# Performance work log

Measured on AMD Instinct MI355X. Metric: run time of the kernel, lower is better.

Reference implementation:

```python
import jax, jax.numpy as jnp
import numpy as np

NUM_PITCHES = 88
H_FEAT = 188
LSTM_UNITS = 48
N_STATES = 5
CTX_HID = 16
CTX_OUT = 4


def _glorot(key, shape):
    fan_in, fan_out = shape[1], shape[0]
    lim = (6.0 / (fan_in + fan_out)) ** 0.5
    return jax.random.uniform(key, shape, jnp.float32, -lim, lim)


def setup_inputs() -> dict:
    key = jax.random.key(0)
    ks = jax.random.split(key, 16)
    B, T = 16, 256
    pitch_features = jax.random.normal(ks[0], (B, NUM_PITCHES, H_FEAT, T), jnp.float32)
    prev_context = jax.random.uniform(ks[1], (B, NUM_PITCHES, 3), jnp.float32)
    # context net params
    fc1_w = _glorot(ks[2], (CTX_HID, 3)); fc1_b = jnp.zeros((CTX_HID,), jnp.float32)
    fc2_w = _glorot(ks[3], (CTX_HID, CTX_HID)); fc2_b = jnp.zeros((CTX_HID,), jnp.float32)
    fc3_w = _glorot(ks[4], (CTX_OUT, CTX_HID)); fc3_b = jnp.zeros((CTX_OUT,), jnp.float32)
    # lstm1: input H_FEAT+4 -> 48; gates order i,f,g,o (torch convention)
    in1 = H_FEAT + CTX_OUT
    lstm1_wih = _glorot(ks[5], (4 * LSTM_UNITS, in1))
    lstm1_whh = _glorot(ks[6], (4 * LSTM_UNITS, LSTM_UNITS))
    lstm1_bih = jnp.zeros((4 * LSTM_UNITS,), jnp.float32)
    lstm1_bhh = jnp.zeros((4 * LSTM_UNITS,), jnp.float32)
    lstm2_wih = _glorot(ks[7], (4 * LSTM_UNITS, LSTM_UNITS))
    lstm2_whh = _glorot(ks[8], (4 * LSTM_UNITS, LSTM_UNITS))
    lstm2_bih = jnp.zeros((4 * LSTM_UNITS,), jnp.float32)
    lstm2_bhh = jnp.zeros((4 * LSTM_UNITS,), jnp.float32)
    fc_states_w = _glorot(ks[9], (N_STATES, LSTM_UNITS))
    fc_states_b = jnp.zeros((N_STATES,), jnp.float32)
    return dict(pitch_features=pitch_features, prev_context=prev_context,
                fc1_w=fc1_w, fc1_b=fc1_b, fc2_w=fc2_w, fc2_b=fc2_b,
                fc3_w=fc3_w, fc3_b=fc3_b,
                lstm1_wih=lstm1_wih, lstm1_whh=lstm1_whh, lstm1_bih=lstm1_bih, lstm1_bhh=lstm1_bhh,
                lstm2_wih=lstm2_wih, lstm2_whh=lstm2_whh, lstm2_bih=lstm2_bih, lstm2_bhh=lstm2_bhh,
                fc_states_w=fc_states_w, fc_states_b=fc_states_b)


def _lstm_scan(x, wih, whh, bih, bhh):
    # x: (S, N, In); zero init state; returns (S, N, U)
    S, N, _ = x.shape
    U = whh.shape[1]
    xg = jnp.einsum('sni,gi->sng', x, wih) + bih + bhh  # precompute input gates

    def step(carry, xg_t):
        h, c = carry
        g = xg_t + h @ whh.T  # (N, 4U)
        i, f, gg, o = jnp.split(g, 4, axis=-1)
        c = jax.nn.sigmoid(f) * c + jax.nn.sigmoid(i) * jnp.tanh(gg)
        h = jax.nn.sigmoid(o) * jnp.tanh(c)
        return (h, c), h

    init = (jnp.zeros((N, U), x.dtype), jnp.zeros((N, U), x.dtype))
    _, hs = jax.lax.scan(step, init, xg)
    return hs


def reference(pitch_features, prev_context,
              fc1_w, fc1_b, fc2_w, fc2_b, fc3_w, fc3_b,
              lstm1_wih, lstm1_whh, lstm1_bih, lstm1_bhh,
              lstm2_wih, lstm2_whh, lstm2_bih, lstm2_bhh,
              fc_states_w, fc_states_b):
    B, P, H, T = pitch_features.shape
    # Context net (context never updates across t in the original loop)
    x = jax.nn.relu(prev_context @ fc1_w.T + fc1_b)
    x = jax.nn.relu(x @ fc2_w.T + fc2_b)
    ctx_emb = x @ fc3_w.T + fc3_b  # (B, P, 4)
    # Each timestep t is independent: LSTM runs over the pitch axis (len 88)
    # with zero initial state every step. Fold (B, T) into batch N.
    pf = jnp.transpose(pitch_features, (1, 0, 3, 2)).reshape(P, B * T, H)  # (P, BT, H)
    ce = jnp.broadcast_to(ctx_emb[:, None, :, :], (B, T, P, CTX_OUT))
    ce = jnp.transpose(ce, (2, 0, 1, 3)).reshape(P, B * T, CTX_OUT)
    seq = jnp.concatenate([pf, ce], axis=-1)  # (P, BT, H+4)
    h = _lstm_scan(seq, lstm1_wih, lstm1_whh, lstm1_bih, lstm1_bhh)
    h = _lstm_scan(h, lstm2_wih, lstm2_whh, lstm2_bih, lstm2_bhh)
    logits = h @ fc_states_w.T + fc_states_b  # (P, BT, 5)
    logits = logits.reshape(P, B, T, N_STATES)
    logits = jnp.transpose(logits, (1, 0, 3, 2))  # (B, P, 5, T)
    return jax.nn.softmax(logits, axis=2)
```

## Files before the change

### kernel.cpp

```cpp
#include <hip/hip_runtime.h>
#include <hip/hip_bf16.h>
#include <cstdint>

#define P_ 88
#define B_ 16
#define T_ 256
#define H_ 188
#define G_ 192
#define U_ 48
#define N_ 4096

typedef __attribute__((ext_vector_type(8))) short bf16x8;
typedef __attribute__((ext_vector_type(8))) _Float16 f16x8;
typedef __attribute__((ext_vector_type(4))) float f32x4;

__device__ __forceinline__ float sigf(float x) {
  return __builtin_amdgcn_rcpf(1.0f + __expf(-x));
}
__device__ __forceinline__ float tanh_f(float x) {
  return 1.0f - 2.0f * __builtin_amdgcn_rcpf(1.0f + __expf(2.0f * x));
}
__device__ __forceinline__ unsigned short f2bs(float v) {
  union { __hip_bfloat16 h; unsigned short s; } u;
  u.h = __float2bfloat16(v);
  return u.s;
}
__device__ __forceinline__ float bs2f(unsigned short s) {
  union { unsigned int u; float f; } x;
  x.u = ((unsigned int)s) << 16;
  return x.f;
}
__device__ __forceinline__ float hs2f(unsigned short s) {
  union { unsigned short u; _Float16 h; } x;
  x.u = s;
  return (float)x.h;
}
__device__ __forceinline__ unsigned short f2hs(float v) {
  union { _Float16 h; unsigned short s; } x;
  x.h = (_Float16)v;
  return x.s;
}

__device__ __forceinline__ void lds_barrier() {
  asm volatile("s_waitcnt lgkmcnt(0)\n\ts_barrier" ::: "memory");
}

__global__ void ctx_kernel(const float* __restrict__ pc,
                           const float* __restrict__ fc1w, const float* __restrict__ fc1b,
                           const float* __restrict__ fc2w, const float* __restrict__ fc2b,
                           const float* __restrict__ fc3w, const float* __restrict__ fc3b,
                           const float* __restrict__ wih1,
                           const float* __restrict__ bih1, const float* __restrict__ bhh1,
                           float* __restrict__ ctxg) {
  int bp = blockIdx.x * 64 + threadIdx.x;
  if (bp >= B_ * P_) return;
  float p0 = pc[bp * 3 + 0], p1 = pc[bp * 3 + 1], p2 = pc[bp * 3 + 2];
  float x1[16], x2[16];
#pragma unroll
  for (int jj = 0; jj < 16; ++jj)
    x1[jj] = fmaxf(0.f, fc1w[jj * 3 + 0] * p0 + fc1w[jj * 3 + 1] * p1 + fc1w[jj * 3 + 2] * p2 + fc1b[jj]);
#pragma unroll
  for (int jj = 0; jj < 16; ++jj) {
    float s = fc2b[jj];
#pragma unroll
    for (int i = 0; i < 16; ++i) s += fc2w[jj * 16 + i] * x1[i];
    x2[jj] = fmaxf(0.f, s);
  }
  float ce[4];
#pragma unroll
  for (int jj = 0; jj < 4; ++jj) {
    float s = fc3b[jj];
#pragma unroll
    for (int i = 0; i < 16; ++i) s += fc3w[jj * 16 + i] * x2[i];
    ce[jj] = s;
  }
  float* op = ctxg + (size_t)bp * G_;
  for (int g = 0; g < G_; ++g) {
    const float* wr = wih1 + (size_t)g * G_ + H_;
    op[g] = bih1[g] + bhh1[g] + ce[0] * wr[0] + ce[1] * wr[1] + ce[2] * wr[2] + ce[3] * wr[3];
  }
}

__global__ __launch_bounds__(256) void wfrag_kernel(const float* __restrict__ wih1,
                                                    f16x8* __restrict__ wfrag) {
  const int idx = blockIdx.x * 256 + threadIdx.x;
  if (idx >= 12 * 6 * 64) return;
  const int l = idx & 63;
  const int kc = (idx >> 6) % 6;
  const int j = idx / 384;
  const int g = j * 16 + (l & 15);
  const int k0 = kc * 32 + (l >> 4) * 8;
  f16x8 v;
#pragma unroll
  for (int e = 0; e < 8; ++e) {
    const int k = k0 + e;
    const float wv = (k < H_) ? wih1[(size_t)g * G_ + k] : 0.f;
    v[e] = (_Float16)wv;
  }
  wfrag[idx] = v;
}

__global__ __launch_bounds__(256, 3) void gemm_mfma(const float* __restrict__ pf,
                                                    const f16x8* __restrict__ wfrag,
                                                    const float* __restrict__ ctxg,
                                                    unsigned short* __restrict__ xg2) {
  const int bp = blockIdx.x >> 1, tb = blockIdx.x & 1;
  const int p = bp % P_, b = bp / P_;
  const int tid = threadIdx.x;
  const int w = tid >> 6, l = tid & 63;
  const int lj = l & 15, lq = l >> 4;

  __shared__ __align__(16) char ldsraw[49152];
  _Float16(*Ahi)[34] = (_Float16(*)[34])ldsraw;
  _Float16(*Alo)[34] = (_Float16(*)[34])(ldsraw + 8704);

  float cg[12];
#pragma unroll
  for (int jn = 0; jn < 12; ++jn)
    cg[jn] = ctxg[(size_t)bp * G_ + jn * 16 + lj];

  f32x4 acc[2][12];
#pragma unroll
  for (int mt = 0; mt < 2; ++mt)
#pragma unroll
    for (int jn = 0; jn < 12; ++jn)
#pragma unroll
      for (int r = 0; r < 4; ++r) acc[mt][jn][r] = 0.f;

  const float* Ab = pf + (size_t)bp * H_ * T_ + tb * 128;
  const int kl = tid >> 5;
  const int t4 = (tid & 31) * 4;

  for (int kc = 0; kc < 6; ++kc) {
    __syncthreads();
#pragma unroll
    for (int rr = 0; rr < 4; ++rr) {
      const int kk = rr * 8 + kl;
      const int kg = kc * 32 + kk;
      float a0 = 0.f, a1 = 0.f, a2 = 0.f, a3 = 0.f;
      if (kg < H_) {
        const float4 v = *(const float4*)(Ab + (size_t)kg * T_ + t4);
        a0 = v.x; a1 = v.y; a2 = v.z; a3 = v.w;
      }
      const _Float16 h0 = (_Float16)a0, h1 = (_Float16)a1;
      const _Float16 h2 = (_Float16)a2, h3 = (_Float16)a3;
      Ahi[t4 + 0][kk] = h0; Alo[t4 + 0][kk] = (_Float16)(a0 - (float)h0);
      Ahi[t4 + 1][kk] = h1; Alo[t4 + 1][kk] = (_Float16)(a1 - (float)h1);
      Ahi[t4 + 2][kk] = h2; Alo[t4 + 2][kk] = (_Float16)(a2 - (float)h2);
      Ahi[t4 + 3][kk] = h3; Alo[t4 + 3][kk] = (_Float16)(a3 - (float)h3);
    }
    __syncthreads();
    const int trow = w * 32;
    const f16x8 ahi0 = *(const f16x8*)&Ahi[trow + lj][lq * 8];
    const f16x8 ahi1 = *(const f16x8*)&Ahi[trow + 16 + lj][lq * 8];
    const f16x8 alo0 = *(const f16x8*)&Alo[trow + lj][lq * 8];
    const f16x8 alo1 = *(const f16x8*)&Alo[trow + 16 + lj][lq * 8];
#pragma unroll
    for (int jn = 0; jn < 12; ++jn) {
      const f16x8 wf = wfrag[(jn * 6 + kc) * 64 + l];
      acc[0][jn] = __builtin_amdgcn_mfma_f32_16x16x32_f16(ahi0, wf, acc[0][jn], 0, 0, 0);
      acc[1][jn] = __builtin_amdgcn_mfma_f32_16x16x32_f16(ahi1, wf, acc[1][jn], 0, 0, 0);
      acc[0][jn] = __builtin_amdgcn_mfma_f32_16x16x32_f16(alo0, wf, acc[0][jn], 0, 0, 0);
      acc[1][jn] = __builtin_amdgcn_mfma_f32_16x16x32_f16(alo1, wf, acc[1][jn], 0, 0, 0);
    }
  }
  __syncthreads();

  unsigned short* Cst = (unsigned short*)ldsraw + w * 6144;
#pragma unroll
  for (int mt = 0; mt < 2; ++mt)
#pragma unroll
    for (int jn = 0; jn < 12; ++jn)
#pragma unroll
      for (int r = 0; r < 4; ++r)
        Cst[mt * 3072 + jn * 256 + r * 64 + l] = f2hs(acc[mt][jn][r] + cg[jn]);
  const int nb0 = b * 16 + tb * 8 + w * 2;
  unsigned short* gb = xg2 + ((size_t)p * 256 + nb0) * 3072;
#pragma unroll
  for (int rr = 0; rr < 12; ++rr) {
    const uint4 v = *(const uint4*)(Cst + rr * 512 + l * 8);
    *(uint4*)(gb + rr * 512 + l * 8) = v;
  }
}

__global__ __launch_bounds__(256, 2) void scan_mfma(
    const unsigned short* __restrict__ xg2,
    const float* __restrict__ whh1, const float* __restrict__ wih2,
    const float* __restrict__ whh2, const float* __restrict__ bih2,
    const float* __restrict__ bhh2, const float* __restrict__ fcw,
    const float* __restrict__ fcb, float* __restrict__ out) {
  __shared__ __align__(16) short hh[16][104];
  __shared__ __align__(16) short hl[16][104];
  __shared__ __align__(16) float gs[8][196];
  __shared__ __align__(16) float h2f[8][52];
  __shared__ __align__(16) float fcws[5 * 48];
  __shared__ float logit_s[5][8];
  __shared__ float prob_s[5][8];

  const int tid = threadIdx.x;
  const int w = tid >> 6;
  const int l = tid & 63;
  const int lj = l & 15;
  const int lq = l >> 4;
  const int grp = blockIdx.x >> 1;
  const int half = blockIdx.x & 1;
  const int n0 = blockIdx.x * 8;
  const int b = n0 >> 8, t0 = n0 & 255;

  bf16x8 b1[3][2];
  bf16x8 b2f[3][3];
  float bias2r[3];
#pragma unroll
  for (int i = 0; i < 3; ++i) {
    const int j = w * 48 + i * 16 + lj;
    bias2r[i] = bih2[j] + bhh2[j];
#pragma unroll
    for (int kc = 0; kc < 2; ++kc)
#pragma unroll
      for (int e = 0; e < 8; ++e) {
        const int u = kc * 32 + lq * 8 + e;
        b1[i][kc][e] = (u < U_) ? (short)f2bs(whh1[j * U_ + u]) : (short)0;
      }
#pragma unroll
    for (int kc = 0; kc < 3; ++kc)
#pragma unroll
      for (int e = 0; e < 8; ++e) {
        const int u = kc * 32 + lq * 8 + e;
        b2f[i][kc][e] = (u < U_) ? (short)f2bs(wih2[j * U_ + u])
                                 : (short)f2bs(whh2[j * U_ + (u - U_)]);
      }
  }

  for (int e = tid; e < 16 * 104 / 2; e += 256) {
    ((unsigned int*)hh)[e] = 0u;
    ((unsigned int*)hl)[e] = 0u;
  }
  for (int e = tid; e < 5 * U_; e += 256) fcws[e] = fcw[e];

  const int tn0 = tid / U_, tu0 = tid % U_;
  const int tn1 = (256 + tid) / U_, tu1 = (256 + tid) % U_;
  float c1r[2] = {0.f, 0.f}, c2r[2] = {0.f, 0.f};
  const bool fcth = tid < 40;
  const int fk = tid >> 3, fn = tid & 7;
  const float fcbr = fcth ? fcb[fk] : 0.f;
  const int sk = (tid - 96) >> 3, sn = (tid - 96) & 7;

  unsigned short xp[12];
  {
    const size_t pb = (size_t)grp * 3072;
#pragma unroll
    for (int i = 0; i < 3; ++i)
#pragma unroll
      for (int r = 0; r < 4; ++r)
        xp[i * 4 + r] = (lq < 2)
            ? xg2[pb + (size_t)((w * 3 + i) * 256 + r * 64 + (half * 2 + lq) * 16 + lj)]
            : (unsigned short)0;
  }
  const short* hhrow = &hh[lj][0];
  const short* hlrow = &hl[lj][0];
  lds_barrier();

  for (int p = 0; p < P_; ++p) {
    f32x4 cH[3], cL[3];
#pragma unroll
    for (int i = 0; i < 3; ++i)
#pragma unroll
      for (int r = 0; r < 4; ++r) { cH[i][r] = hs2f(xp[i * 4 + r]); cL[i][r] = 0.f; }
    if (p < P_ - 1) {
      const size_t pb = (size_t)((p + 1) * 256 + grp) * 3072;
#pragma unroll
      for (int i = 0; i < 3; ++i)
#pragma unroll
        for (int r = 0; r < 4; ++r)
          xp[i * 4 + r] = (lq < 2)
              ? xg2[pb + (size_t)((w * 3 + i) * 256 + r * 64 + (half * 2 + lq) * 16 + lj)]
              : (unsigned short)0;
    }
    {
      bf16x8 ah0 = *(const bf16x8*)(hhrow + lq * 8);
      bf16x8 ah1 = *(const bf16x8*)(hhrow + 32 + lq * 8);
      bf16x8 al0 = *(const bf16x8*)(hlrow + lq * 8);
      bf16x8 al1 = *(const bf16x8*)(hlrow + 32 + lq * 8);
#pragma unroll
      for (int i = 0; i < 3; ++i)
        cH[i] = __builtin_amdgcn_mfma_f32_16x16x32_bf16(ah0, b1[i][0], cH[i], 0, 0, 0);
#pragma unroll
      for (int i = 0; i < 3; ++i)
        cL[i] = __builtin_amdgcn_mfma_f32_16x16x32_bf16(al0, b1[i][0], cL[i], 0, 0, 0);
#pragma unroll
      for (int i = 0; i < 3; ++i)
        cH[i] = __builtin_amdgcn_mfma_f32_16x16x32_bf16(ah1, b1[i][1], cH[i], 0, 0, 0);
#pragma unroll
      for (int i = 0; i < 3; ++i)
        cL[i] = __builtin_amdgcn_mfma_f32_16x16x32_bf16(al1, b1[i][1], cL[i], 0, 0, 0);
    }
    if (lq < 2) {
#pragma unroll
      for (int i = 0; i < 3; ++i)
#pragma unroll
        for (int r = 0; r < 4; ++r)
          gs[lq * 4 + r][w * 48 + i * 16 + lj] = cH[i][r] + cL[i][r];
    }
    if (p > 0 && fcth) {
      float a = fcbr;
#pragma unroll
      for (int uq = 0; uq < 12; ++uq) {
        f32x4 hv = *(const f32x4*)&h2f[fn][uq * 4];
        f32x4 wv = *(const f32x4*)&fcws[fk * 48 + uq * 4];
        a += hv[0] * wv[0] + hv[1] * wv[1] + hv[2] * wv[2] + hv[3] * wv[3];
      }
      logit_s[fk][fn] = a;
    }
    lds_barrier();
    {
      const int n = tn0, u = tu0;
      const float ig = gs[n][u], fg = gs[n][48 + u];
      const float gg = gs[n][96 + u], og = gs[n][144 + u];
      const float cc = sigf(fg) * c1r[0] + sigf(ig) * tanh_f(gg);
      c1r[0] = cc;
      const float h = sigf(og) * tanh_f(cc);
      const unsigned short hb = f2bs(h);
      hh[n][u] = (short)hb;
      hl[n][u] = (short)f2bs(h - bs2f(hb));
    }
    if (tid < 128) {
      const int n = tn1, u = tu1;
      const float ig = gs[n][u], fg = gs[n][48 + u];
      const float gg = gs[n][96 + u], og = gs[n][144 + u];
      const float cc = sigf(fg) * c1r[1] + sigf(ig) * tanh_f(gg);
      c1r[1] = cc;
      const float h = sigf(og) * tanh_f(cc);
      const unsigned short hb = f2bs(h);
      hh[n][u] = (short)hb;
      hl[n][u] = (short)f2bs(h - bs2f(hb));
    }
    if (p > 0 && tid >= 192 && tid < 200) {
      const int n = tid - 192;
      const float l0 = logit_s[0][n], l1 = logit_s[1][n], l2 = logit_s[2][n],
                  l3 = logit_s[3][n], l4 = logit_s[4][n];
      const float m = fmaxf(fmaxf(fmaxf(l0, l1), fmaxf(l2, l3)), l4);
      const float e0 = __expf(l0 - m), e1 = __expf(l1 - m), e2 = __expf(l2 - m),
                  e3 = __expf(l3 - m), e4 = __expf(l4 - m);
      const float rs = __builtin_amdgcn_rcpf(e0 + e1 + e2 + e3 + e4);
      prob_s[0][n] = e0 * rs; prob_s[1][n] = e1 * rs; prob_s[2][n] = e2 * rs;
      prob_s[3][n] = e3 * rs; prob_s[4][n] = e4 * rs;
    }
    lds_barrier();
    f32x4 c2H[3], c2L[3];
#pragma unroll
    for (int i = 0; i < 3; ++i) {
      c2H[i][0] = bias2r[i]; c2H[i][1] = bias2r[i];
      c2H[i][2] = bias2r[i]; c2H[i][3] = bias2r[i];
      c2L[i][0] = 0.f; c2L[i][1] = 0.f; c2L[i][2] = 0.f; c2L[i][3] = 0.f;
    }
    {
      bf16x8 a0 = *(const bf16x8*)(hhrow + lq * 8);
      bf16x8 a1 = *(const bf16x8*)(hhrow + 32 + lq * 8);
      bf16x8 a2 = *(const bf16x8*)(hhrow + 64 + lq * 8);
      bf16x8 q0 = *(const bf16x8*)(hlrow + lq * 8);
      bf16x8 q1 = *(const bf16x8*)(hlrow + 32 + lq * 8);
      bf16x8 q2 = *(const bf16x8*)(hlrow + 64 + lq * 8);
#pragma unroll
      for (int i = 0; i < 3; ++i)
        c2H[i] = __builtin_amdgcn_mfma_f32_16x16x32_bf16(a0, b2f[i][0], c2H[i], 0, 0, 0);
#pragma unroll
      for (int i = 0; i < 3; ++i)
        c2L[i] = __builtin_amdgcn_mfma_f32_16x16x32_bf16(q0, b2f[i][0], c2L[i], 0, 0, 0);
#pragma unroll
      for (int i = 0; i < 3; ++i)
        c2H[i] = __builtin_amdgcn_mfma_f32_16x16x32_bf16(a1, b2f[i][1], c2H[i], 0, 0, 0);
#pragma unroll
      for (int i = 0; i < 3; ++i)
        c2L[i] = __builtin_amdgcn_mfma_f32_16x16x32_bf16(q1, b2f[i][1], c2L[i], 0, 0, 0);
#pragma unroll
      for (int i = 0; i < 3; ++i)
        c2H[i] = __builtin_amdgcn_mfma_f32_16x16x32_bf16(a2, b2f[i][2], c2H[i], 0, 0, 0);
#pragma unroll
      for (int i = 0; i < 3; ++i)
        c2L[i] = __builtin_amdgcn_mfma_f32_16x16x32_bf16(q2, b2f[i][2], c2L[i], 0, 0, 0);
    }
    if (lq < 2) {
#pragma unroll
      for (int i = 0; i < 3; ++i)
#pragma unroll
        for (int r = 0; r < 4; ++r)
          gs[lq * 4 + r][w * 48 + i * 16 + lj] = c2H[i][r] + c2L[i][r];
    }
    if (p > 0 && tid >= 96 && tid < 136) {
      out[(((size_t)b * P_ + (p - 1)) * 5 + sk) * T_ + t0 + sn] = prob_s[sk][sn];
    }
    lds_barrier();
    {
      const int n = tn0, u = tu0;
      const float ig = gs[n][u], fg = gs[n][48 + u];
      const float gg = gs[n][96 + u], og = gs[n][144 + u];
      const float cc = sigf(fg) * c2r[0] + sigf(ig) * tanh_f(gg);
      c2r[0] = cc;
      const float h = sigf(og) * tanh_f(cc);
      const unsigned short hb = f2bs(h);
      hh[n][48 + u] = (short)hb;
      hl[n][48 + u] = (short)f2bs(h - bs2f(hb));
      h2f[n][u] = h;
    }
    if (tid < 128) {
      const int n = tn1, u = tu1;
      const float ig = gs[n][u], fg = gs[n][48 + u];
      const float gg = gs[n][96 + u], og = gs[n][144 + u];
      const float cc = sigf(fg) * c2r[1] + sigf(ig) * tanh_f(gg);
      c2r[1] = cc;
      const float h = sigf(og) * tanh_f(cc);
      const unsigned short hb = f2bs(h);
      hh[n][48 + u] = (short)hb;
      hl[n][48 + u] = (short)f2bs(h - bs2f(hb));
      h2f[n][u] = h;
    }
    lds_barrier();
  }
  if (fcth) {
    float a = fcbr;
#pragma unroll
    for (int uq = 0; uq < 12; ++uq) {
      f32x4 hv = *(const f32x4*)&h2f[fn][uq * 4];
      f32x4 wv = *(const f32x4*)&fcws[fk * 48 + uq * 4];
      a += hv[0] * wv[0] + hv[1] * wv[1] + hv[2] * wv[2] + hv[3] * wv[3];
    }
    logit_s[fk][fn] = a;
  }
  lds_barrier();
  if (tid >= 192 && tid < 200) {
    const int n = tid - 192;
    const float l0 = logit_s[0][n], l1 = logit_s[1][n], l2 = logit_s[2][n],
                l3 = logit_s[3][n], l4 = logit_s[4][n];
    const float m = fmaxf(fmaxf(fmaxf(l0, l1), fmaxf(l2, l3)), l4);
    const float e0 = __expf(l0 - m), e1 = __expf(l1 - m), e2 = __expf(l2 - m),
                e3 = __expf(l3 - m), e4 = __expf(l4 - m);
    const float rs = __builtin_amdgcn_rcpf(e0 + e1 + e2 + e3 + e4);
    prob_s[0][n] = e0 * rs; prob_s[1][n] = e1 * rs; prob_s[2][n] = e2 * rs;
    prob_s[3][n] = e3 * rs; prob_s[4][n] = e4 * rs;
  }
  lds_barrier();
  if (tid >= 96 && tid < 136) {
    out[(((size_t)b * P_ + (P_ - 1)) * 5 + sk) * T_ + t0 + sn] = prob_s[sk][sn];
  }
}

extern "C" void kernel_launch(void* const* d_in, const int* in_sizes, int n_in,
                              void* d_out, int out_size, void* d_ws, size_t ws_size,
                              hipStream_t stream) {
  const float* pf   = (const float*)d_in[0];
  const float* pc   = (const float*)d_in[1];
  const float* fc1w = (const float*)d_in[2];
  const float* fc1b = (const float*)d_in[3];
  const float* fc2w = (const float*)d_in[4];
  const float* fc2b = (const float*)d_in[5];
  const float* fc3w = (const float*)d_in[6];
  const float* fc3b = (const float*)d_in[7];
  const float* wih1 = (const float*)d_in[8];
  const float* whh1 = (const float*)d_in[9];
  const float* bih1 = (const float*)d_in[10];
  const float* bhh1 = (const float*)d_in[11];
  const float* wih2 = (const float*)d_in[12];
  const float* whh2 = (const float*)d_in[13];
  const float* bih2 = (const float*)d_in[14];
  const float* bhh2 = (const float*)d_in[15];
  const float* fcw  = (const float*)d_in[16];
  const float* fcb  = (const float*)d_in[17];
  float* out = (float*)d_out;

  char* wsp = (char*)d_ws;
  float* ctxg = (float*)wsp;
  const size_t CTXG_BYTES = (size_t)B_ * P_ * G_ * sizeof(float);
  f16x8* wfrag = (f16x8*)(wsp + CTXG_BYTES);
  const size_t WFRAG_BYTES = (size_t)12 * 6 * 64 * 16;
  unsigned short* xg2 = (unsigned short*)(wsp + CTXG_BYTES + WFRAG_BYTES);

  ctx_kernel<<<22, 64, 0, stream>>>(pc, fc1w, fc1b, fc2w, fc2b, fc3w, fc3b,
                                    wih1, bih1, bhh1, ctxg);
  wfrag_kernel<<<18, 256, 0, stream>>>(wih1, wfrag);
  gemm_mfma<<<B_ * P_ * 2, 256, 0, stream>>>(pf, wfrag, ctxg, xg2);
  scan_mfma<<<N_ / 8, 256, 0, stream>>>(xg2, whh1, wih2, whh2,
                                        bih2, bhh2, fcw, fcb, out);
}
```

Measured before the change: 413.2 us.

## Process two 8-sequence groups per scan block to interleave independent recurrences

```diff
diff --git a/kernel.cpp b/kernel.cpp
--- a/kernel.cpp
+++ b/kernel.cpp
@@ -39,6 +39,14 @@
   union { _Float16 h; unsigned short s; } x;
   x.h = (_Float16)v;
   return x.s;
+}
+__device__ __forceinline__ void hsplit(float h, unsigned short& hi, unsigned short& lo) {
+  union { float f; unsigned int u; } x;
+  x.f = h;
+  hi = (unsigned short)(x.u >> 16);
+  union { float f; unsigned int u; } y;
+  y.f = h - bs2f(hi);
+  lo = (unsigned short)(y.u >> 16);
 }
 
 __device__ __forceinline__ void lds_barrier() {
@@ -183,28 +191,27 @@
   }
 }
 
-__global__ __launch_bounds__(256, 2) void scan_mfma(
+__global__ __launch_bounds__(256, 1) void scan_mfma(
     const unsigned short* __restrict__ xg2,
     const float* __restrict__ whh1, const float* __restrict__ wih2,
     const float* __restrict__ whh2, const float* __restrict__ bih2,
     const float* __restrict__ bhh2, const float* __restrict__ fcw,
     const float* __restrict__ fcb, float* __restrict__ out) {
-  __shared__ __align__(16) short hh[16][104];
-  __shared__ __align__(16) short hl[16][104];
-  __shared__ __align__(16) float gs[8][196];
-  __shared__ __align__(16) float h2f[8][52];
+  __shared__ __align__(16) short hhX[16][104], hlX[16][104];
+  __shared__ __align__(16) short hhY[16][104], hlY[16][104];
+  __shared__ __align__(16) float gsX[8][196], gsY[8][196];
+  __shared__ __align__(16) float h2fX[8][52], h2fY[8][52];
   __shared__ __align__(16) float fcws[5 * 48];
-  __shared__ float logit_s[5][8];
-  __shared__ float prob_s[5][8];
+  __shared__ float logitX[5][8], probX[5][8];
+  __shared__ float logitY[5][8], probY[5][8];
 
   const int tid = threadIdx.x;
   const int w = tid >> 6;
   const int l = tid & 63;
   const int lj = l & 15;
   const int lq = l >> 4;
-  const int grp = blockIdx.x >> 1;
-  const int half = blockIdx.x & 1;
-  const int n0 = blockIdx.x * 8;
+  const int grp = blockIdx.x;
+  const int n0 = grp * 16;
   const int b = n0 >> 8, t0 = n0 & 255;
 
   bf16x8 b1[3][2];
@@ -232,215 +239,360 @@
   }
 
   for (int e = tid; e < 16 * 104 / 2; e += 256) {
-    ((unsigned int*)hh)[e] = 0u;
-    ((unsigned int*)hl)[e] = 0u;
+    ((unsigned int*)hhX)[e] = 0u; ((unsigned int*)hlX)[e] = 0u;
+    ((unsigned int*)hhY)[e] = 0u; ((unsigned int*)hlY)[e] = 0u;
   }
   for (int e = tid; e < 5 * U_; e += 256) fcws[e] = fcw[e];
 
   const int tn0 = tid / U_, tu0 = tid % U_;
   const int tn1 = (256 + tid) / U_, tu1 = (256 + tid) % U_;
-  float c1r[2] = {0.f, 0.f}, c2r[2] = {0.f, 0.f};
-  const bool fcth = tid < 40;
-  const int fk = tid >> 3, fn = tid & 7;
-  const float fcbr = fcth ? fcb[fk] : 0.f;
-  const int sk = (tid - 96) >> 3, sn = (tid - 96) & 7;
-
-  unsigned short xp[12];
+  float c1X[2] = {0.f, 0.f}, c1Y[2] = {0.f, 0.f};
+  float c2X[2] = {0.f, 0.f}, c2Y[2] = {0.f, 0.f};
+
+  const bool fcXth = tid < 40, fcYth = tid >= 40 && tid < 80;
+  const int fi = fcXth ? tid : (tid - 40);
+  const int fk = fi >> 3, fn = fi & 7;
+  const float fcbr = (fcXth || fcYth) ? fcb[fk] : 0.f;
+  const bool stXth = tid >= 96 && tid < 136, stYth = tid >= 136 && tid < 176;
+  const int si = stXth ? (tid - 96) : (tid - 136);
+  const int sk = si >> 3, sn = si & 7;
+  const bool smXth = tid >= 192 && tid < 200, smYth = tid >= 200 && tid < 208;
+  const int smn = smXth ? (tid - 192) : (tid - 200);
+
+  unsigned short xpX[12], xpY[12];
   {
     const size_t pb = (size_t)grp * 3072;
 #pragma unroll
     for (int i = 0; i < 3; ++i)
 #pragma unroll
-      for (int r = 0; r < 4; ++r)
-        xp[i * 4 + r] = (lq < 2)
-            ? xg2[pb + (size_t)((w * 3 + i) * 256 + r * 64 + (half * 2 + lq) * 16 + lj)]
-            : (unsigned short)0;
-  }
-  const short* hhrow = &hh[lj][0];
-  const short* hlrow = &hl[lj][0];
+      for (int r = 0; r < 4; ++r) {
+        const size_t base = pb + (size_t)((w * 3 + i) * 256 + r * 64);
+        xpX[i * 4 + r] = (lq < 2) ? xg2[base + lq * 16 + lj] : (unsigned short)0;
+        xpY[i * 4 + r] = (lq < 2) ? xg2[base + (2 + lq) * 16 + lj] : (unsigned short)0;
+      }
+  }
   lds_barrier();
 
   for (int p = 0; p < P_; ++p) {
-    f32x4 cH[3], cL[3];
+    f32x4 cHX[3], cLX[3], cHY[3], cLY[3];
 #pragma unroll
     for (int i = 0; i < 3; ++i)
 #pragma unroll
-      for (int r = 0; r < 4; ++r) { cH[i][r] = hs2f(xp[i * 4 + r]); cL[i][r] = 0.f; }
+      for (int r = 0; r < 4; ++r) {
+        cHX[i][r] = hs2f(xpX[i * 4 + r]); cLX[i][r] = 0.f;
+        cHY[i][r] = hs2f(xpY[i * 4 + r]); cLY[i][r] = 0.f;
+      }
     if (p < P_ - 1) {
       const size_t pb = (size_t)((p + 1) * 256 + grp) * 3072;
 #pragma unroll
       for (int i = 0; i < 3; ++i)
 #pragma unroll
-        for (int r = 0; r < 4; ++r)
-          xp[i * 4 + r] = (lq < 2)
-              ? xg2[pb + (size_t)((w * 3 + i) * 256 + r * 64 + (half * 2 + lq) * 16 + lj)]
-              : (unsigned short)0;
+        for (int r = 0; r < 4; ++r) {
+          const size_t base = pb + (size_t)((w * 3 + i) * 256 + r * 64);
+          xpX[i * 4 + r] = (lq < 2) ? xg2[base + lq * 16 + lj] : (unsigned short)0;
+          xpY[i * 4 + r] = (lq < 2) ? xg2[base + (2 + lq) * 16 + lj] : (unsigned short)0;
+        }
     }
     {
-      bf16x8 ah0 = *(const bf16x8*)(hhrow + lq * 8);
-      bf16x8 ah1 = *(const bf16x8*)(hhrow + 32 + lq * 8);
-      bf16x8 al0 = *(const bf16x8*)(hlrow + lq * 8);
-      bf16x8 al1 = *(const bf16x8*)(hlrow + 32 + lq * 8);
+      const short* hrX = &hhX[lj][0];
+      const short* lrX = &hlX[lj][0];
+      const short* hrY = &hhY[lj][0];
+      const short* lrY = &hlY[lj][0];
+      bf16x8 xa0 = *(const bf16x8*)(hrX + lq * 8);
+      bf16x8 xa1 = *(const bf16x8*)(hrX + 32 + lq * 8);
+      bf16x8 xl0 = *(const bf16x8*)(lrX + lq * 8);
+      bf16x8 xl1 = *(const bf16x8*)(lrX + 32 + lq * 8);
+      bf16x8 ya0 = *(const bf16x8*)(hrY + lq * 8);
+      bf16x8 ya1 = *(const bf16x8*)(hrY + 32 + lq * 8);
+      bf16x8 yl0 = *(const bf16x8*)(lrY + lq * 8);
+      bf16x8 yl1 = *(const bf16x8*)(lrY + 32 + lq * 8);
+#pragma unroll
+      for (int i = 0; i < 3; ++i) {
+        cHX[i] = __builtin_amdgcn_mfma_f32_16x16x32_bf16(xa0, b1[i][0], cHX[i], 0, 0, 0);
+        cHY[i] = __builtin_amdgcn_mfma_f32_16x16x32_bf16(ya0, b1[i][0], cHY[i], 0, 0, 0);
+      }
+#pragma unroll
+      for (int i = 0; i < 3; ++i) {
+        cLX[i] = __builtin_amdgcn_mfma_f32_16x16x32_bf16(xl0, b1[i][0], cLX[i], 0, 0, 0);
+        cLY[i] = __builtin_amdgcn_mfma_f32_16x16x32_bf16(yl0, b1[i][0], cLY[i], 0, 0, 0);
+      }
+#pragma unroll
+      for (int i = 0; i < 3; ++i) {
+        cHX[i] = __builtin_amdgcn_mfma_f32_16x16x32_bf16(xa1, b1[i][1], cHX[i], 0, 0, 0);
+        cHY[i] = __builtin_amdgcn_mfma_f32_16x16x32_bf16(ya1, b1[i][1], cHY[i], 0, 0, 0);
+      }
+#pragma unroll
+      for (int i = 0; i < 3; ++i) {
+        cLX[i] = __builtin_amdgcn_mfma_f32_16x16x32_bf16(xl1, b1[i][1], cLX[i], 0, 0, 0);
+        cLY[i] = __builtin_amdgcn_mfma_f32_16x16x32_bf16(yl1, b1[i][1], cLY[i], 0, 0, 0);
+      }
+    }
+    if (lq < 2) {
 #pragma unroll
       for (int i = 0; i < 3; ++i)
-        cH[i] = __builtin_amdgcn_mfma_f32_16x16x32_bf16(ah0, b1[i][0], cH[i], 0, 0, 0);
-#pragma unroll
-      for (int i = 0; i < 3; ++i)
-        cL[i] = __builtin_amdgcn_mfma_f32_16x16x32_bf16(al0, b1[i][0], cL[i], 0, 0, 0);
-#pragma unroll
-      for (int i = 0; i < 3; ++i)
-        cH[i] = __builtin_amdgcn_mfma_f32_16x16x32_bf16(ah1, b1[i][1], cH[i], 0, 0, 0);
-#pragma unroll
-      for (int i = 0; i < 3; ++i)
-        cL[i] = __builtin_amdgcn_mfma_f32_16x16x32_bf16(al1, b1[i][1], cL[i], 0, 0, 0);
-    }
-    if (lq < 2) {
-#pragma unroll
-      for (int i = 0; i < 3; ++i)
-#pragma unroll
-        for (int r = 0; r < 4; ++r)
-          gs[lq * 4 + r][w * 48 + i * 16 + lj] = cH[i][r] + cL[i][r];
-    }
-    if (p > 0 && fcth) {
+#pragma unroll
+        for (int r = 0; r < 4; ++r) {
+          gsX[lq * 4 + r][w * 48 + i * 16 + lj] = cHX[i][r] + cLX[i][r];
+          gsY[lq * 4 + r][w * 48 + i * 16 + lj] = cHY[i][r] + cLY[i][r];
+        }
+    }
+    if (p > 0 && fcXth) {
       float a = fcbr;
 #pragma unroll
       for (int uq = 0; uq < 12; ++uq) {
-        f32x4 hv = *(const f32x4*)&h2f[fn][uq * 4];
+        f32x4 hv = *(const f32x4*)&h2fX[fn][uq * 4];
         f32x4 wv = *(const f32x4*)&fcws[fk * 48 + uq * 4];
         a += hv[0] * wv[0] + hv[1] * wv[1] + hv[2] * wv[2] + hv[3] * wv[3];
       }
-      logit_s[fk][fn] = a;
+      logitX[fk][fn] = a;
+    }
+    if (p > 0 && fcYth) {
+      float a = fcbr;
+#pragma unroll
+      for (int uq = 0; uq < 12; ++uq) {
+        f32x4 hv = *(const f32x4*)&h2fY[fn][uq * 4];
+        f32x4 wv = *(const f32x4*)&fcws[fk * 48 + uq * 4];
+        a += hv[0] * wv[0] + hv[1] * wv[1] + hv[2] * wv[2] + hv[3] * wv[3];
+      }
+      logitY[fk][fn] = a;
     }
     lds_barrier();
     {
       const int n = tn0, u = tu0;
-      const float ig = gs[n][u], fg = gs[n][48 + u];
-      const float gg = gs[n][96 + u], og = gs[n][144 + u];
-      const float cc = sigf(fg) * c1r[0] + sigf(ig) * tanh_f(gg);
-      c1r[0] = cc;
-      const float h = sigf(og) * tanh_f(cc);
-      const unsigned short hb = f2bs(h);
-      hh[n][u] = (short)hb;
-      hl[n][u] = (short)f2bs(h - bs2f(hb));
+      {
+        const float ig = gsX[n][u], fg = gsX[n][48 + u];
+        const float gg = gsX[n][96 + u], og = gsX[n][144 + u];
+        const float cc = sigf(fg) * c1X[0] + sigf(ig) * tanh_f(gg);
+        c1X[0] = cc;
+        const float h = sigf(og) * tanh_f(cc);
+        unsigned short hb, lb; hsplit(h, hb, lb);
+        hhX[n][u] = (short)hb; hlX[n][u] = (short)lb;
+      }
+      {
+        const float ig = gsY[n][u], fg = gsY[n][48 + u];
+        const float gg = gsY[n][96 + u], og = gsY[n][144 + u];
+        const float cc = sigf(fg) * c1Y[0] + sigf(ig) * tanh_f(gg);
+        c1Y[0] = cc;
+        const float h = sigf(og) * tanh_f(cc);
+        unsigned short hb, lb; hsplit(h, hb, lb);
+        hhY[n][u] = (short)hb; hlY[n][u] = (short)lb;
+      }
     }
     if (tid < 128) {
       const int n = tn1, u = tu1;
-      const float ig = gs[n][u], fg = gs[n][48 + u];
-      const float gg = gs[n][96 + u], og = gs[n][144 + u];
-      const float cc = sigf(fg) * c1r[1] + sigf(ig) * tanh_f(gg);
-      c1r[1] = cc;
-      const float h = sigf(og) * tanh_f(cc);
-      const unsigned short hb = f2bs(h);
-      hh[n][u] = (short)hb;
-      hl[n][u] = (short)f2bs(h - bs2f(hb));
-    }
-    if (p > 0 && tid >= 192 && tid < 200) {
-      const int n = tid - 192;
-      const float l0 = logit_s[0][n], l1 = logit_s[1][n], l2 = logit_s[2][n],
-                  l3 = logit_s[3][n], l4 = logit_s[4][n];
+      {
+        const float ig = gsX[n][u], fg = gsX[n][48 + u];
+        const float gg = gsX[n][96 + u], og = gsX[n][144 + u];
+        const float cc = sigf(fg) * c1X[1] + sigf(ig) * tanh_f(gg);
+        c1X[1] = cc;
+        const float h = sigf(og) * tanh_f(cc);
+        unsigned short hb, lb; hsplit(h, hb, lb);
+        hhX[n][u] = (short)hb; hlX[n][u] = (short)lb;
+      }
+      {
+        const float ig = gsY[n][u], fg = gsY[n][48 + u];
+        const float gg = gsY[n][96 + u], og = gsY[n][144 + u];
+        const float cc = sigf(fg) * c1Y[1] + sigf(ig) * tanh_f(gg);
+        c1Y[1] = cc;
+        const float h = sigf(og) * tanh_f(cc);
+        unsigned short hb, lb; hsplit(h, hb, lb);
+        hhY[n][u] = (short)hb; hlY[n][u] = (short)lb;
+      }
+    }
+    if (p > 0 && smXth) {
+      const int n = smn;
+      const float l0 = logitX[0][n], l1 = logitX[1][n], l2 = logitX[2][n],
+                  l3 = logitX[3][n], l4 = logitX[4][n];
       const float m = fmaxf(fmaxf(fmaxf(l0, l1), fmaxf(l2, l3)), l4);
       const float e0 = __expf(l0 - m), e1 = __expf(l1 - m), e2 = __expf(l2 - m),
                   e3 = __expf(l3 - m), e4 = __expf(l4 - m);
       const float rs = __builtin_amdgcn_rcpf(e0 + e1 + e2 + e3 + e4);
-      prob_s[0][n] = e0 * rs; prob_s[1][n] = e1 * rs; prob_s[2][n] = e2 * rs;
-      prob_s[3][n] = e3 * rs; prob_s[4][n] = e4 * rs;
+      probX[0][n] = e0 * rs; probX[1][n] = e1 * rs; probX[2][n] = e2 * rs;
+      probX[3][n] = e3 * rs; probX[4][n] = e4 * rs;
+    }
+    if (p > 0 && smYth) {
+      const int n = smn;
+      const float l0 = logitY[0][n], l1 = logitY[1][n], l2 = logitY[2][n],
+                  l3 = logitY[3][n], l4 = logitY[4][n];
+      const float m = fmaxf(fmaxf(fmaxf(l0, l1), fmaxf(l2, l3)), l4);
+      const float e0 = __expf(l0 - m), e1 = __expf(l1 - m), e2 = __expf(l2 - m),
+                  e3 = __expf(l3 - m), e4 = __expf(l4 - m);
+      const float rs = __builtin_amdgcn_rcpf(e0 + e1 + e2 + e3 + e4);
+      probY[0][n] = e0 * rs; probY[1][n] = e1 * rs; probY[2][n] = e2 * rs;
+      probY[3][n] = e3 * rs; probY[4][n] = e4 * rs;
     }
     lds_barrier();
-    f32x4 c2H[3], c2L[3];
+    f32x4 dHX[3], dLX[3], dHY[3], dLY[3];
 #pragma unroll
     for (int i = 0; i < 3; ++i) {
-      c2H[i][0] = bias2r[i]; c2H[i][1] = bias2r[i];
-      c2H[i][2] = bias2r[i]; c2H[i][3] = bias2r[i];
-      c2L[i][0] = 0.f; c2L[i][1] = 0.f; c2L[i][2] = 0.f; c2L[i][3] = 0.f;
+      dHX[i][0] = bias2r[i]; dHX[i][1] = bias2r[i];
+      dHX[i][2] = bias2r[i]; dHX[i][3] = bias2r[i];
+      dHY[i][0] = bias2r[i]; dHY[i][1] = bias2r[i];
+      dHY[i][2] = bias2r[i]; dHY[i][3] = bias2r[i];
+      dLX[i][0] = 0.f; dLX[i][1] = 0.f; dLX[i][2] = 0.f; dLX[i][3] = 0.f;
+      dLY[i][0] = 0.f; dLY[i][1] = 0.f; dLY[i][2] = 0.f; dLY[i][3] = 0.f;
     }
     {
-      bf16x8 a0 = *(const bf16x8*)(hhrow + lq * 8);
-      bf16x8 a1 = *(const bf16x8*)(hhrow + 32 + lq * 8);
-      bf16x8 a2 = *(const bf16x8*)(hhrow + 64 + lq * 8);
-      bf16x8 q0 = *(const bf16x8*)(hlrow + lq * 8);
-      bf16x8 q1 = *(const bf16x8*)(hlrow + 32 + lq * 8);
-      bf16x8 q2 = *(const bf16x8*)(hlrow + 64 + lq * 8);
+      const short* hrX = &hhX[lj][0];
+      const short* lrX = &hlX[lj][0];
+      const short* hrY = &hhY[lj][0];
+      const short* lrY = &hlY[lj][0];
+      bf16x8 xa0 = *(const bf16x8*)(hrX + lq * 8);
+      bf16x8 xa1 = *(const bf16x8*)(hrX + 32 + lq * 8);
+      bf16x8 xa2 = *(const bf16x8*)(hrX + 64 + lq * 8);
+      bf16x8 xq0 = *(const bf16x8*)(lrX + lq * 8);
+      bf16x8 xq1 = *(const bf16x8*)(lrX + 32 + lq * 8);
+      bf16x8 xq2 = *(const bf16x8*)(lrX + 64 + lq * 8);
+      bf16x8 ya0 = *(const bf16x8*)(hrY + lq * 8);
+      bf16x8 ya1 = *(const bf16x8*)(hrY + 32 + lq * 8);
+      bf16x8 ya2 = *(const bf16x8*)(hrY + 64 + lq * 8);
+      bf16x8 yq0 = *(const bf16x8*)(lrY + lq * 8);
+      bf16x8 yq1 = *(const bf16x8*)(lrY + 32 + lq * 8);
+      bf16x8 yq2 = *(const bf16x8*)(lrY + 64 + lq * 8);
+#pragma unroll
+      for (int i = 0; i < 3; ++i) {
+        dHX[i] = __builtin_amdgcn_mfma_f32_16x16x32_bf16(xa0, b2f[i][0], dHX[i], 0, 0, 0);
+        dHY[i] = __builtin_amdgcn_mfma_f32_16x16x32_bf16(ya0, b2f[i][0], dHY[i], 0, 0, 0);
+      }
+#pragma unroll
+      for (int i = 0; i < 3; ++i) {
+        dLX[i] = __builtin_amdgcn_mfma_f32_16x16x32_bf16(xq0, b2f[i][0], dLX[i], 0, 0, 0);
+        dLY[i] = __builtin_amdgcn_mfma_f32_16x16x32_bf16(yq0, b2f[i][0], dLY[i], 0, 0, 0);
+      }
+#pragma unroll
+      for (int i = 0; i < 3; ++i) {
+        dHX[i] = __builtin_amdgcn_mfma_f32_16x16x32_bf16(xa1, b2f[i][1], dHX[i], 0, 0, 0);
+        dHY[i] = __builtin_amdgcn_mfma_f32_16x16x32_bf16(ya1, b2f[i][1], dHY[i], 0, 0, 0);
+      }
+#pragma unroll
+      for (int i = 0; i < 3; ++i) {
+        dLX[i] = __builtin_amdgcn_mfma_f32_16x16x32_bf16(xq1, b2f[i][1], dLX[i], 0, 0, 0);
+        dLY[i] = __builtin_amdgcn_mfma_f32_16x16x32_bf16(yq1, b2f[i][1], dLY[i], 0, 0, 0);
+      }
+#pragma unroll
+      for (int i = 0; i < 3; ++i) {
+        dHX[i] = __builtin_amdgcn_mfma_f32_16x16x32_bf16(xa2, b2f[i][2], dHX[i], 0, 0, 0);
+        dHY[i] = __builtin_amdgcn_mfma_f32_16x16x32_bf16(ya2, b2f[i][2], dHY[i], 0, 0, 0);
+      }
+#pragma unroll
+      for (int i = 0; i < 3; ++i) {
+        dLX[i] = __builtin_amdgcn_mfma_f32_16x16x32_bf16(xq2, b2f[i][2], dLX[i], 0, 0, 0);
+        dLY[i] = __builtin_amdgcn_mfma_f32_16x16x32_bf16(yq2, b2f[i][2], dLY[i], 0, 0, 0);
+      }
+    }
+    if (lq < 2) {
 #pragma unroll
       for (int i = 0; i < 3; ++i)
-        c2H[i] = __builtin_amdgcn_mfma_f32_16x16x32_bf16(a0, b2f[i][0], c2H[i], 0, 0, 0);
-#pragma unroll
-      for (int i = 0; i < 3; ++i)
-        c2L[i] = __builtin_amdgcn_mfma_f32_16x16x32_bf16(q0, b2f[i][0], c2L[i], 0, 0, 0);
-#pragma unroll
-      for (int i = 0; i < 3; ++i)
-        c2H[i] = __builtin_amdgcn_mfma_f32_16x16x32_bf16(a1, b2f[i][1], c2H[i], 0, 0, 0);
-#pragma unroll
-      for (int i = 0; i < 3; ++i)
-        c2L[i] = __builtin_amdgcn_mfma_f32_16x16x32_bf16(q1, b2f[i][1], c2L[i], 0, 0, 0);
-#pragma unroll
-      for (int i = 0; i < 3; ++i)
-        c2H[i] = __builtin_amdgcn_mfma_f32_16x16x32_bf16(a2, b2f[i][2], c2H[i], 0, 0, 0);
-#pragma unroll
-      for (int i = 0; i < 3; ++i)
-        c2L[i] = __builtin_amdgcn_mfma_f32_16x16x32_bf16(q2, b2f[i][2], c2L[i], 0, 0, 0);
-    }
-    if (lq < 2) {
-#pragma unroll
-      for (int i = 0; i < 3; ++i)
-#pragma unroll
-        for (int r = 0; r < 4; ++r)
-          gs[lq * 4 + r][w * 48 + i * 16 + lj] = c2H[i][r] + c2L[i][r];
-    }
-    if (p > 0 && tid >= 96 && tid < 136) {
-      out[(((size_t)b * P_ + (p - 1)) * 5 + sk) * T_ + t0 + sn] = prob_s[sk][sn];
+#pragma unroll
+        for (int r = 0; r < 4; ++r) {
+          gsX[lq * 4 + r][w * 48 + i * 16 + lj] = dHX[i][r] + dLX[i][r];
+          gsY[lq * 4 + r][w * 48 + i * 16 + lj] = dHY[i][r] + dLY[i][r];
+        }
+    }
+    if (p > 0 && stXth) {
+      out[(((size_t)b * P_ + (p - 1)) * 5 + sk) * T_ + t0 + sn] = probX[sk][sn];
+    }
+    if (p > 0 && stYth) {
+      out[(((size_t)b * P_ + (p - 1)) * 5 + sk) * T_ + t0 + 8 + sn] = probY[sk][sn];
     }
     lds_barrier();
     {
       const int n = tn0, u = tu0;
-      const float ig = gs[n][u], fg = gs[n][48 + u];
-      const float gg = gs[n][96 + u], og = gs[n][144 + u];
-      const float cc = sigf(fg) * c2r[0] + sigf(ig) * tanh_f(gg);
-      c2r[0] = cc;
-      const float h = sigf(og) * tanh_f(cc);
-      const unsigned short hb = f2bs(h);
-      hh[n][48 + u] = (short)hb;
-      hl[n][48 + u] = (short)f2bs(h - bs2f(hb));
-      h2f[n][u] = h;
+      {
+        const float ig = gsX[n][u], fg = gsX[n][48 + u];
+        const float gg = gsX[n][96 + u], og = gsX[n][144 + u];
+        const float cc = sigf(fg) * c2X[0] + sigf(ig) * tanh_f(gg);
+        c2X[0] = cc;
+        const float h = sigf(og) * tanh_f(cc);
+        unsigned short hb, lb; hsplit(h, hb, lb);
+        hhX[n][48 + u] = (short)hb; hlX[n][48 + u] = (short)lb;
+        h2fX[n][u] = h;
+      }
+      {
+        const float ig = gsY[n][u], fg = gsY[n][48 + u];
+        const float gg = gsY[n][96 + u], og = gsY[n][144 + u];
+        const float cc = sigf(fg) * c2Y[0] + sigf(ig) * tanh_f(gg);
+        c2Y[0] = cc;
+        const float h = sigf(og) * tanh_f(cc);
+        unsigned short hb, lb; hsplit(h, hb, lb);
+        hhY[n][48 + u] = (short)hb; hlY[n][48 + u] = (short)lb;
+        h2fY[n][u] = h;
+      }
     }
     if (tid < 128) {
       const int n = tn1, u = tu1;
-      const float ig = gs[n][u], fg = gs[n][48 + u];
-      const float gg = gs[n][96 + u], og = gs[n][144 + u];
-      const float cc = sigf(fg) * c2r[1] + sigf(ig) * tanh_f(gg);
-      c2r[1] = cc;
-      const float h = sigf(og) * tanh_f(cc);
-      const unsigned short hb = f2bs(h);
-      hh[n][48 + u] = (short)hb;
-      hl[n][48 + u] = (short)f2bs(h - bs2f(hb));
-      h2f[n][u] = h;
+      {
+        const float ig = gsX[n][u], fg = gsX[n][48 + u];
+        const float gg = gsX[n][96 + u], og = gsX[n][144 + u];
+        const float cc = sigf(fg) * c2X[1] + sigf(ig) * tanh_f(gg);
+        c2X[1] = cc;
+        const float h = sigf(og) * tanh_f(cc);
+        unsigned short hb, lb; hsplit(h, hb, lb);
+        hhX[n][48 + u] = (short)hb; hlX[n][48 + u] = (short)lb;
+        h2fX[n][u] = h;
+      }
+      {
+        const float ig = gsY[n][u], fg = gsY[n][48 + u];
+        const float gg = gsY[n][96 + u], og = gsY[n][144 + u];
+        const float cc = sigf(fg) * c2Y[1] + sigf(ig) * tanh_f(gg);
+        c2Y[1] = cc;
+        const float h = sigf(og) * tanh_f(cc);
+        unsigned short hb, lb; hsplit(h, hb, lb);
+        hhY[n][48 + u] = (short)hb; hlY[n][48 + u] = (short)lb;
+        h2fY[n][u] = h;
+      }
     }
     lds_barrier();
   }
-  if (fcth) {
+  if (fcXth) {
     float a = fcbr;
 #pragma unroll
     for (int uq = 0; uq < 12; ++uq) {
-      f32x4 hv = *(const f32x4*)&h2f[fn][uq * 4];
+      f32x4 hv = *(const f32x4*)&h2fX[fn][uq * 4];
       f32x4 wv = *(const f32x4*)&fcws[fk * 48 + uq * 4];
       a += hv[0] * wv[0] + hv[1] * wv[1] + hv[2] * wv[2] + hv[3] * wv[3];
     }
-    logit_s[fk][fn] = a;
+    logitX[fk][fn] = a;
+  }
+  if (fcYth) {
+    float a = fcbr;
+#pragma unroll
+    for (int uq = 0; uq < 12; ++uq) {
+      f32x4 hv = *(const f32x4*)&h2fY[fn][uq * 4];
+      f32x4 wv = *(const f32x4*)&fcws[fk * 48 + uq * 4];
+      a += hv[0] * wv[0] + hv[1] * wv[1] + hv[2] * wv[2] + hv[3] * wv[3];
+    }
+    logitY[fk][fn] = a;
   }
   lds_barrier();
-  if (tid >= 192 && tid < 200) {
-    const int n = tid - 192;
-    const float l0 = logit_s[0][n], l1 = logit_s[1][n], l2 = logit_s[2][n],
-                l3 = logit_s[3][n], l4 = logit_s[4][n];
+  if (smXth) {
+    const int n = smn;
+    const float l0 = logitX[0][n], l1 = logitX[1][n], l2 = logitX[2][n],
+                l3 = logitX[3][n], l4 = logitX[4][n];
     const float m = fmaxf(fmaxf(fmaxf(l0, l1), fmaxf(l2, l3)), l4);
     const float e0 = __expf(l0 - m), e1 = __expf(l1 - m), e2 = __expf(l2 - m),
                 e3 = __expf(l3 - m), e4 = __expf(l4 - m);
     const float rs = __builtin_amdgcn_rcpf(e0 + e1 + e2 + e3 + e4);
-    prob_s[0][n] = e0 * rs; prob_s[1][n] = e1 * rs; prob_s[2][n] = e2 * rs;
-    prob_s[3][n] = e3 * rs; prob_s[4][n] = e4 * rs;
+    probX[0][n] = e0 * rs; probX[1][n] = e1 * rs; probX[2][n] = e2 * rs;
+    probX[3][n] = e3 * rs; probX[4][n] = e4 * rs;
+  }
+  if (smYth) {
+    const int n = smn;
+    const float l0 = logitY[0][n], l1 = logitY[1][n], l2 = logitY[2][n],
+                l3 = logitY[3][n], l4 = logitY[4][n];
+    const float m = fmaxf(fmaxf(fmaxf(l0, l1), fmaxf(l2, l3)), l4);
+    const float e0 = __expf(l0 - m), e1 = __expf(l1 - m), e2 = __expf(l2 - m),
+                e3 = __expf(l3 - m), e4 = __expf(l4 - m);
+    const float rs = __builtin_amdgcn_rcpf(e0 + e1 + e2 + e3 + e4);
+    probY[0][n] = e0 * rs; probY[1][n] = e1 * rs; probY[2][n] = e2 * rs;
+    probY[3][n] = e3 * rs; probY[4][n] = e4 * rs;
   }
   lds_barrier();
-  if (tid >= 96 && tid < 136) {
-    out[(((size_t)b * P_ + (P_ - 1)) * 5 + sk) * T_ + t0 + sn] = prob_s[sk][sn];
+  if (stXth) {
+    out[(((size_t)b * P_ + (P_ - 1)) * 5 + sk) * T_ + t0 + sn] = probX[sk][sn];
+  }
+  if (stYth) {
+    out[(((size_t)b * P_ + (P_ - 1)) * 5 + sk) * T_ + t0 + 8 + sn] = probY[sk][sn];
   }
 }
 
@@ -478,6 +630,6 @@
                                     wih1, bih1, bhh1, ctxg);
   wfrag_kernel<<<18, 256, 0, stream>>>(wih1, wfrag);
   gemm_mfma<<<B_ * P_ * 2, 256, 0, stream>>>(pf, wfrag, ctxg, xg2);
-  scan_mfma<<<N_ / 8, 256, 0, stream>>>(xg2, whh1, wih2, whh2,
-                                        bih2, bhh2, fcw, fcb, out);
-}
+  scan_mfma<<<N_ / 16, 256, 0, stream>>>(xg2, whh1, wih2, whh2,
+                                         bih2, bhh2, fcw, fcb, out);
+}
```

Result: slower. 525.7 us (+27.2%).
